# Performance work log

Measured on AMD Instinct MI355X. Metric: run time of the kernel, lower is better.

## Reference

```python
import jax, jax.numpy as jnp
import numpy as np

B, S, D, H, DC, HC, M = 2, 2048, 1024, 16, 64, 16, 4096
DH = D // H  # head_dim = 64


def _ln(x, g, b, eps=1e-5):
    m = jnp.mean(x, axis=-1, keepdims=True)
    v = jnp.var(x, axis=-1, keepdims=True)
    return (x - m) * jax.lax.rsqrt(v + eps) * g + b


def setup_inputs() -> dict:
    key = jax.random.key(0)
    ks = jax.random.split(key, 10)
    def w(k, shape, fan_in):
        return jax.random.normal(k, shape, jnp.float32) * (fan_in ** -0.5)
    return {
        "h": jax.random.normal(ks[0], (B, S, D), jnp.float32),
        "z": jax.random.normal(ks[1], (B, S, DC), jnp.float32),
        # Linear weights stored [in, out] (transpose of torch layout)
        "wv": w(ks[2], (D, D), D),   "bv": jnp.zeros((D,), jnp.float32),
        "wca": w(ks[3], (DC, H * HC), DC), "bca": jnp.zeros((H * HC,), jnp.float32),
        "wcn": w(ks[4], (D, DC), D), "bcn": jnp.zeros((DC,), jnp.float32),
        "wo": w(ks[5], (D, D), D),   "bo": jnp.zeros((D,), jnp.float32),
        "gamma": jnp.zeros((1, H, 1, 1), jnp.float32),
        "w1": w(ks[6], (D, M), D),   "b1": jnp.zeros((M,), jnp.float32),
        "w2": w(ks[7], (M, D), M),   "b2": jnp.zeros((D,), jnp.float32),
        "ln1_g": jnp.ones((D,), jnp.float32),  "ln1_b": jnp.zeros((D,), jnp.float32),
        "ln2_g": jnp.ones((D,), jnp.float32),  "ln2_b": jnp.zeros((D,), jnp.float32),
        "lnc_g": jnp.ones((DC,), jnp.float32), "lnc_b": jnp.zeros((DC,), jnp.float32),
    }


def reference(h, z, wv, bv, wca, bca, wcn, bcn, wo, bo, gamma,
              w1, b1, w2, b2, ln1_g, ln1_b, ln2_g, ln2_b, lnc_g, lnc_b):
    hn = _ln(h, ln1_g, ln1_b)
    # values: [B,S,H,DH]
    value = (hn @ wv + bv).reshape(B, S, H, DH)
    # per-head coordinates: [B,S,H,HC]
    zh = (z @ wca + bca).reshape(B, S, H, HC)
    # pairwise squared distances per head: ||zq||^2 + ||zk||^2 - 2 zq.zk
    z_sq = jnp.sum(zh * zh, axis=-1).transpose(0, 2, 1)        # [B,H,S]
    dot = jnp.einsum('bqhc,bkhc->bhqk', zh, zh)                # [B,H,S,S]
    sq_dist = jnp.maximum(z_sq[:, :, :, None] + z_sq[:, :, None, :] - 2.0 * dot, 0.0)
    g = jax.nn.softplus(gamma)                                 # [1,H,1,1]
    attn = jax.nn.softmax(-g * sq_dist, axis=-1)               # [B,H,S,S]
    attn_out = jnp.einsum('bhqk,bkhd->bqhd', attn, value).reshape(B, S, D)
    h_attn = attn_out @ wo + bo
    z_next = hn @ wcn + bcn
    h = h + h_attn
    # FFN (dropout is identity in eval); torch GELU default is exact (erf)
    hn2 = _ln(h, ln2_g, ln2_b)
    ffn = jax.nn.gelu(hn2 @ w1 + b1, approximate=False) @ w2 + b2
    h = h + ffn
    z_out = _ln(z + z_next, lnc_g, lnc_b)
    return h, z_out
```

## Files before the change

### kernel.cpp

```cpp
#include <hip/hip_runtime.h>

#define USH unsigned short

__device__ __forceinline__ float b2f(USH u) {
    union { unsigned int i; float f; } x; x.i = ((unsigned int)u) << 16; return x.f;
}
__device__ __forceinline__ USH f2b(float f) {
    union { float f; unsigned int i; } x; x.f = f;
    unsigned int r = x.i + (0x7fffu + ((x.i >> 16) & 1u));
    return (USH)(r >> 16);
}
__device__ __forceinline__ float ldf(const USH* p)  { return b2f(*p); }
__device__ __forceinline__ float ldf(const float* p){ return *p; }
__device__ __forceinline__ void stf(USH* p, float v)  { *p = f2b(v); }
__device__ __forceinline__ void stf(float* p, float v){ *p = v; }

#define GLOAD16(gp, lp) __builtin_amdgcn_global_load_lds(                     \
    (const __attribute__((address_space(1))) void*)(gp),                      \
    (__attribute__((address_space(3))) void*)(lp), 16, 0, 0)

typedef __attribute__((ext_vector_type(8))) __bf16 bf16x8;
typedef __attribute__((ext_vector_type(4))) float  floatx4;

__global__ __launch_bounds__(256) void transpose_f2b(const float* __restrict__ W,
                                                     USH* __restrict__ WT,
                                                     int K, int N) {
    __shared__ USH t[64][72];
    int n0 = blockIdx.x * 64, k0 = blockIdx.y * 64;
    int tid = threadIdx.x;
    int kr = tid >> 4, nc = (tid & 15) * 4;
#pragma unroll
    for (int r = 0; r < 4; r++) {
        int k = kr + r * 16;
        float4 v = *(const float4*)(W + (size_t)(k0 + k) * N + n0 + nc);
        t[nc + 0][k] = f2b(v.x); t[nc + 1][k] = f2b(v.y);
        t[nc + 2][k] = f2b(v.z); t[nc + 3][k] = f2b(v.w);
    }
    __syncthreads();
    int nr = tid >> 2, kc = (tid & 3) * 8;
#pragma unroll
    for (int r = 0; r < 2; r++) {
        int k = kc + r * 32;
        *(int4*)(WT + (size_t)(n0 + nr) * K + k0 + k) = *(const int4*)&t[nr][k];
    }
}

template <typename TX>
__global__ __launch_bounds__(256) void ln_rows(const TX* __restrict__ x,
                                               const float* __restrict__ g,
                                               const float* __restrict__ bb,
                                               USH* __restrict__ y) {
    int row = blockIdx.x, tid = threadIdx.x;
    const TX* xr = x + (size_t)row * 1024 + tid * 4;
    float v[4];
#pragma unroll
    for (int i = 0; i < 4; i++) v[i] = ldf(xr + i);
    float s  = v[0] + v[1] + v[2] + v[3];
    float ss = v[0]*v[0] + v[1]*v[1] + v[2]*v[2] + v[3]*v[3];
#pragma unroll
    for (int o = 32; o; o >>= 1) { s += __shfl_down(s, o); ss += __shfl_down(ss, o); }
    __shared__ float red[10];
    int w = tid >> 6;
    if ((tid & 63) == 0) { red[w] = s; red[4 + w] = ss; }
    __syncthreads();
    if (tid == 0) {
        float S = red[0] + red[1] + red[2] + red[3];
        float SS = red[4] + red[5] + red[6] + red[7];
        float mean = S * (1.f / 1024.f);
        float var  = SS * (1.f / 1024.f) - mean * mean;
        red[8] = mean; red[9] = rsqrtf(var + 1e-5f);
    }
    __syncthreads();
    float mean = red[8], rstd = red[9];
    USH* yr = y + (size_t)row * 1024 + tid * 4;
#pragma unroll
    for (int i = 0; i < 4; i++) {
        int c = tid * 4 + i;
        yr[i] = f2b((v[i] - mean) * rstd * g[c] + bb[c]);
    }
}

__global__ __launch_bounds__(256) void zh_kernel(const float* __restrict__ z,
                                                 const float* __restrict__ wca,
                                                 const float* __restrict__ bca,
                                                 const float* __restrict__ gamma,
                                                 USH* __restrict__ zq_pack,
                                                 USH* __restrict__ zk_pack) {
    int row = blockIdx.x, n = threadIdx.x;
    __shared__ float zrow[64];
    if (n < 64) zrow[n] = z[(size_t)row * 64 + n];
    __syncthreads();
    float s = bca[n];
#pragma unroll 8
    for (int k = 0; k < 64; k++) s = fmaf(zrow[k], wca[(size_t)k * 256 + n], s);
    int h = n >> 4, c = n & 15;
    float gvl = log1pf(__expf(gamma[h])) * 1.44269504f;
    USH u = f2b(s);
    float sv = b2f(u);
    float sq = sv * sv;
    sq += __shfl_xor(sq, 1); sq += __shfl_xor(sq, 2);
    sq += __shfl_xor(sq, 4); sq += __shfl_xor(sq, 8);
    size_t base = ((size_t)h * 4096 + row) * 32;
    zk_pack[base + c] = u;
    zq_pack[base + c] = f2b(2.f * gvl * s);
    if (c == 0) {
        USH hi = f2b(sq);
        float lo = sq - b2f(hi);
        unsigned int kw0 = 0x3F80u | ((unsigned int)hi << 16);
        unsigned int kw1 = (unsigned int)f2b(lo);
        uint4 kv = {kw0, kw1, 0u, 0u};
        uint4 zz = {0u, 0u, 0u, 0u};
        *(uint4*)(zk_pack + base + 16) = kv;
        *(uint4*)(zk_pack + base + 24) = zz;
        unsigned int qw0 = (unsigned int)f2b(-gvl * sq) | ((unsigned int)f2b(-gvl) << 16);
        unsigned int qw1 = (unsigned int)f2b(-gvl);
        uint4 qv = {qw0, qw1, 0u, 0u};
        *(uint4*)(zq_pack + base + 16) = qv;
        *(uint4*)(zq_pack + base + 24) = zz;
    }
}

template <int EPI, int MI, int NI, int KB, typename TRES, typename TOUT>
__global__ __launch_bounds__(256) void gemm_kernel(const USH* __restrict__ A,
                                                   const USH* __restrict__ WT,
                                                   const float* __restrict__ bias,
                                                   const TRES* __restrict__ res,
                                                   TOUT* __restrict__ out,
                                                   int M, int N, int K) {
    constexpr int BM  = MI * 32;
    constexpr int BN  = NI * 32;
    constexpr int GR  = KB / 8;
    constexpr int RPC = 2048 / KB;
    constexpr int ACH = BM / RPC;
    constexpr int BCH = BN / RPC;
    __shared__ __align__(16) USH lA[BM][KB];
    __shared__ __align__(16) USH lB[BN][KB];
    int tid = threadIdx.x;
    int lane = tid & 63, wave = tid >> 6;
    int wr = wave >> 1, wc = wave & 1;
    int quad = lane >> 4, l15 = lane & 15;
    int m0 = blockIdx.x * BM, n0 = blockIdx.y * BN;

    int srow = tid / GR;
    int kg   = tid % GR;
    int scol = (kg ^ (srow & 7)) * 8;

    const USH* gA = A + (size_t)(m0 + srow) * K + scol;
    const USH* gB = WT + (size_t)(n0 + srow) * K + scol;
    USH* lA0 = &lA[0][0] + tid * 8;
    USH* lB0 = &lB[0][0] + tid * 8;
    int xo = (l15 & 7) * 8;

    floatx4 acc[MI][NI] = {};

    for (int k0 = 0; k0 < K; k0 += KB) {
#pragma unroll
        for (int c = 0; c < ACH; c++)
            GLOAD16(gA + (size_t)c * RPC * K + k0, lA0 + c * 2048);
#pragma unroll
        for (int c = 0; c < BCH; c++)
            GLOAD16(gB + (size_t)c * RPC * K + k0, lB0 + c * 2048);
        __syncthreads();

#pragma unroll
        for (int ks = 0; ks < KB / 32; ks++) {
            bf16x8 bfr[NI];
#pragma unroll
            for (int ni = 0; ni < NI; ni++)
                bfr[ni] = *(const bf16x8*)&lB[wc * (NI * 16) + ni * 16 + l15][(ks * 32 + quad * 8) ^ xo];
#pragma unroll
            for (int mi = 0; mi < MI; mi++) {
                bf16x8 afr = *(const bf16x8*)&lA[wr * (MI * 16) + mi * 16 + l15][(ks * 32 + quad * 8) ^ xo];
#pragma unroll
                for (int ni = 0; ni < NI; ni++)
                    acc[mi][ni] = __builtin_amdgcn_mfma_f32_16x16x32_bf16(afr, bfr[ni], acc[mi][ni], 0, 0, 0);
            }
        }
        __syncthreads();
    }

    float bias_v[NI];
#pragma unroll
    for (int ni = 0; ni < NI; ni++) bias_v[ni] = bias[n0 + wc * (NI * 16) + ni * 16 + l15];

#pragma unroll
    for (int mi = 0; mi < MI; mi++) {
#pragma unroll
        for (int r = 0; r < 4; r++) {
            int row = m0 + wr * (MI * 16) + mi * 16 + quad * 4 + r;
            size_t base = (size_t)row * N;
#pragma unroll
            for (int ni = 0; ni < NI; ni++) {
                int col = n0 + wc * (NI * 16) + ni * 16 + l15;
                float v = acc[mi][ni][r] + bias_v[ni];
                if (EPI == 2) {
                    float t = v * v;
                    float a = fmaf(t, -0.0713548162726f, -1.59576912161f);
                    v = v * __builtin_amdgcn_rcpf(1.f + __expf(v * a));
                }
                if (EPI == 1 || EPI == 3) v += ldf(res + base + col);
                stf(out + base + col, v);
            }
        }
    }
}

__global__ __launch_bounds__(512) void attn11_kernel(const USH* __restrict__ zq_pack,
                                                     const USH* __restrict__ zk_pack,
                                                     const USH* __restrict__ value,
                                                     USH* __restrict__ attn_out) {
    int b = blockIdx.x >> 4, h = blockIdx.x & 15;
    int q0 = blockIdx.y * 128;
    int tid = threadIdx.x, lane = tid & 63, wq = tid >> 6;
    int quad = lane >> 4, l15 = lane & 15;

    __shared__ __align__(16) USH Qb[128][40];
    __shared__ __align__(16) USH KbT[2][64][40];
    __shared__ __align__(16) USH VbT[2][64][72];
    __shared__ __align__(16) USH Pb[8][16][72];

    const size_t zrow0 = (size_t)b * 2048;
    const USH* zq = zq_pack + ((size_t)h * 4096 + zrow0) * 32;
    const USH* zk = zk_pack + ((size_t)h * 4096 + zrow0) * 32;
    const size_t vbase = zrow0 * 1024 + h * 64;

    {
        int row = tid >> 2, c0 = (tid & 3) * 8;
        *(uint4*)&Qb[row][c0] = *(const uint4*)(zq + (size_t)(q0 + row) * 32 + c0);
    }
    __syncthreads();

    bf16x8 afragQ = *(const bf16x8*)&Qb[wq * 16 + l15][quad * 8];

    union { unsigned int u[4]; bf16x8 v; } onesu;
#pragma unroll
    for (int i = 0; i < 4; i++) onesu.u[i] = 0x3F803F80u;
    bf16x8 ones = onesu.v;

    floatx4 oacc[4] = {};
    floatx4 lacc = {};

    int kp  = tid & 31;
    int va  = kp & 15, vb = kp >> 4;
    int vrow = va + vb * 32;
    int dh0  = (tid >> 5) * 8;
    int cb   = va * 4 + vb * 2;
    int krow = (tid - 256) >> 2, kc0 = ((tid - 256) & 3) * 8;
    int4 vta, vtb; uint4 kreg;

    if (tid < 256) {
        const USH* s0 = value + vbase + (size_t)vrow * 1024 + dh0;
        vta = *(const int4*)s0;
        vtb = *(const int4*)(s0 + 16 * 1024);
        const USH* ua = (const USH*)&vta;
        const USH* ub = (const USH*)&vtb;
#pragma unroll
        for (int e = 0; e < 8; e++) {
            unsigned int dw = (unsigned int)ua[e] | ((unsigned int)ub[e] << 16);
            *(unsigned int*)&VbT[0][dh0 + e][cb] = dw;
        }
        const USH* s1 = value + vbase + (size_t)(64 + vrow) * 1024 + dh0;
        vta = *(const int4*)s1;
        vtb = *(const int4*)(s1 + 16 * 1024);
    } else {
        kreg = *(const uint4*)(zk + (size_t)krow * 32 + kc0);
        *(uint4*)&KbT[0][krow][kc0] = kreg;
        kreg = *(const uint4*)(zk + (size_t)(64 + krow) * 32 + kc0);
    }

    for (int it = 0; it < 32; it++) {
        int cur = it & 1;
        __syncthreads();
        if (it + 1 < 32) {
            if (tid < 256) {
                const USH* ua = (const USH*)&vta;
                const USH* ub = (const USH*)&vtb;
#pragma unroll
                for (int e = 0; e < 8; e++) {
                    unsigned int dw = (unsigned int)ua[e] | ((unsigned int)ub[e] << 16);
                    *(unsigned int*)&VbT[cur ^ 1][dh0 + e][cb] = dw;
                }
                if (it + 2 < 32) {
                    const USH* s0 = value + vbase + (size_t)((it + 2) * 64 + vrow) * 1024 + dh0;
                    vta = *(const int4*)s0;
                    vtb = *(const int4*)(s0 + 16 * 1024);
                }
            } else {
                *(uint4*)&KbT[cur ^ 1][krow][kc0] = kreg;
                if (it + 2 < 32)
                    kreg = *(const uint4*)(zk + (size_t)((it + 2) * 64 + krow) * 32 + kc0);
            }
        }

        bf16x8 bk[4];
#pragma unroll
        for (int ni = 0; ni < 4; ni++)
            bk[ni] = *(const bf16x8*)&KbT[cur][ni * 16 + l15][quad * 8];

        floatx4 sacc[4];
#pragma unroll
        for (int ni = 0; ni < 4; ni++) {
            floatx4 zz = {};
            sacc[ni] = __builtin_amdgcn_mfma_f32_16x16x32_bf16(afragQ, bk[ni], zz, 0, 0, 0);
        }

#pragma unroll
        for (int r = 0; r < 4; r++) {
            union { float f; unsigned int i; } c0, c1, c2, c3;
            c0.f = exp2f(sacc[0][r]); c1.f = exp2f(sacc[1][r]);
            c2.f = exp2f(sacc[2][r]); c3.f = exp2f(sacc[3][r]);
            uint2 dw;
            dw.x = (c0.i >> 16) | (c1.i & 0xFFFF0000u);
            dw.y = (c2.i >> 16) | (c3.i & 0xFFFF0000u);
            *(uint2*)&Pb[wq][quad * 4 + r][l15 * 4] = dw;
        }

#pragma unroll
        for (int ks2 = 0; ks2 < 2; ks2++) {
            bf16x8 bv[4];
#pragma unroll
            for (int nd = 0; nd < 4; nd++)
                bv[nd] = *(const bf16x8*)&VbT[cur][nd * 16 + l15][ks2 * 32 + quad * 8];
            bf16x8 ap = *(const bf16x8*)&Pb[wq][l15][ks2 * 32 + quad * 8];
#pragma unroll
            for (int nd = 0; nd < 4; nd++)
                oacc[nd] = __builtin_amdgcn_mfma_f32_16x16x32_bf16(ap, bv[nd], oacc[nd], 0, 0, 0);
            lacc = __builtin_amdgcn_mfma_f32_16x16x32_bf16(ap, ones, lacc, 0, 0, 0);
        }
    }

#pragma unroll
    for (int r = 0; r < 4; r++) {
        float inv = 1.f / lacc[r];
        int row = q0 + wq * 16 + quad * 4 + r;
        USH* o = attn_out + (zrow0 + row) * 1024 + h * 64;
#pragma unroll
        for (int nd = 0; nd < 4; nd++) o[nd * 16 + l15] = f2b(oacc[nd][r] * inv);
    }
}

__global__ __launch_bounds__(64) void lnc_kernel(const float* __restrict__ z,
                                                 const float* __restrict__ zn,
                                                 const float* __restrict__ g,
                                                 const float* __restrict__ bb,
                                                 float* __restrict__ out) {
    int row = blockIdx.x, t = threadIdx.x;
    float v = z[(size_t)row * 64 + t] + zn[(size_t)row * 64 + t];
    float s = v, ss = v * v;
#pragma unroll
    for (int o = 32; o; o >>= 1) { s += __shfl_xor(s, o); ss += __shfl_xor(ss, o); }
    float mean = s * (1.f / 64.f);
    float rstd = rsqrtf(ss * (1.f / 64.f) - mean * mean + 1e-5f);
    out[(size_t)row * 64 + t] = (v - mean) * rstd * g[t] + bb[t];
}

extern "C" void kernel_launch(void* const* d_in, const int* in_sizes, int n_in,
                              void* d_out, int out_size, void* d_ws, size_t ws_size,
                              hipStream_t stream) {
    char* p = (char*)d_ws;
    USH*   value   = (USH*)(p);
    USH*   attn_o  = (USH*)(p + ((size_t)8  << 20));
    USH*   wcnT    = (USH*)(p + ((size_t)8  << 20));
    USH*   zq_pack = (USH*)(p + ((size_t)16 << 20));
    USH*   zk_pack = (USH*)(p + ((size_t)20 << 20));
    USH*   hn      = (USH*)(p + ((size_t)24 << 20));
    USH*   mid     = (USH*)(p);
    USH*   hn2     = (USH*)(p + ((size_t)32 << 20));
    float* znext   = (float*)(p + ((size_t)40 << 20));
    USH*   wvT     = (USH*)(p + ((size_t)41 << 20));
    USH*   woT     = (USH*)(p + ((size_t)43 << 20));
    USH*   w1T     = (USH*)(p + ((size_t)45 << 20));
    USH*   w2T     = (USH*)(p + ((size_t)53 << 20));

    const float *h    = (const float*)d_in[0],  *z    = (const float*)d_in[1];
    const float *wv   = (const float*)d_in[2],  *bv   = (const float*)d_in[3];
    const float *wca  = (const float*)d_in[4],  *bca  = (const float*)d_in[5];
    const float *wcn  = (const float*)d_in[6],  *bcn  = (const float*)d_in[7];
    const float *wo   = (const float*)d_in[8],  *bo   = (const float*)d_in[9];
    const float *gam  = (const float*)d_in[10];
    const float *w1   = (const float*)d_in[11], *b1   = (const float*)d_in[12];
    const float *w2   = (const float*)d_in[13], *b2   = (const float*)d_in[14];
    const float *ln1g = (const float*)d_in[15], *ln1b = (const float*)d_in[16];
    const float *ln2g = (const float*)d_in[17], *ln2b = (const float*)d_in[18];
    const float *lncg = (const float*)d_in[19], *lncb = (const float*)d_in[20];

    float* out_h = (float*)d_out;
    float* out_z = out_h + (size_t)4096 * 1024;
    float* h1    = out_h;

    transpose_f2b<<<dim3(16, 16), 256, 0, stream>>>(wv, wvT, 1024, 1024);
    transpose_f2b<<<dim3(16, 16), 256, 0, stream>>>(wo, woT, 1024, 1024);
    transpose_f2b<<<dim3(64, 16), 256, 0, stream>>>(w1, w1T, 1024, 4096);
    transpose_f2b<<<dim3(16, 64), 256, 0, stream>>>(w2, w2T, 4096, 1024);
    transpose_f2b<<<dim3(1, 16),  256, 0, stream>>>(wcn, wcnT, 1024, 64);

    ln_rows<float><<<4096, 256, 0, stream>>>(h, ln1g, ln1b, hn);
    zh_kernel<<<4096, 256, 0, stream>>>(z, wca, bca, gam, zq_pack, zk_pack);
    gemm_kernel<0, 4, 2, 128, USH, USH><<<dim3(32, 16), 256, 0, stream>>>(hn, wvT, bv, (const USH*)nullptr, value, 4096, 1024, 1024);
    gemm_kernel<0, 1, 1, 64, float, float><<<dim3(128, 2), 256, 0, stream>>>(hn, wcnT, bcn, (const float*)nullptr, znext, 4096, 64, 1024);
    attn11_kernel<<<dim3(32, 16), 512, 0, stream>>>(zq_pack, zk_pack, value, attn_o);
    gemm_kernel<1, 4, 2, 128, float, float><<<dim3(32, 16), 256, 0, stream>>>(attn_o, woT, bo, h, h1, 4096, 1024, 1024);
    ln_rows<float><<<4096, 256, 0, stream>>>(h1, ln2g, ln2b, hn2);
    gemm_kernel<2, 4, 4, 64, USH, USH><<<dim3(32, 32), 256, 0, stream>>>(hn2, w1T, b1, (const USH*)nullptr, mid, 4096, 4096, 1024);
    gemm_kernel<3, 4, 2, 128, float, float><<<dim3(32, 16), 256, 0, stream>>>(mid, w2T, b2, h1, out_h, 4096, 1024, 4096);
    lnc_kernel<<<4096, 64, 0, stream>>>(z, znext, lncg, lncb, out_z);
}
```

Baseline: 353.9 us.

## Split attention key tiles across warp groups and merge partial sums in LDS

The attention kernel now handles 64 queries per block instead of 128, doubling the grid. Within each block, two warp groups each process half of every 64-key tile, and their partial output and denominator accumulators are summed through shared memory at the end. The V transpose layout is changed to match, and shared memory is reused for the merge buffer. The aim is more blocks to fill the CUs and shorter dependent MFMA chains per wave. The cost is that each query block streams K and V from global memory, so total K/V loading doubles, plus an extra LDS reduction step.

```diff
diff --git a/kernel.cpp b/kernel.cpp
--- a/kernel.cpp
+++ b/kernel.cpp
@@ -205,32 +205,31 @@
     }
 }
 
-__global__ __launch_bounds__(512) void attn11_kernel(const USH* __restrict__ zq_pack,
+__global__ __launch_bounds__(512) void attn12_kernel(const USH* __restrict__ zq_pack,
                                                      const USH* __restrict__ zk_pack,
                                                      const USH* __restrict__ value,
                                                      USH* __restrict__ attn_out) {
     int b = blockIdx.x >> 4, h = blockIdx.x & 15;
-    int q0 = blockIdx.y * 128;
+    int q0 = blockIdx.y * 64;
     int tid = threadIdx.x, lane = tid & 63, wq = tid >> 6;
+    int qw = wq & 3, kg = wq >> 2;
     int quad = lane >> 4, l15 = lane & 15;
 
-    __shared__ __align__(16) USH Qb[128][40];
-    __shared__ __align__(16) USH KbT[2][64][40];
-    __shared__ __align__(16) USH VbT[2][64][72];
-    __shared__ __align__(16) USH Pb[8][16][72];
+    __shared__ __align__(16) char smem[38912];
+    typedef USH VbT_t[64][72];
+    typedef USH KbT_t[64][40];
+    typedef USH Pb_t[16][40];
+    VbT_t* VbT = reinterpret_cast<VbT_t*>(smem);
+    KbT_t* KbT = reinterpret_cast<KbT_t*>(smem + 18432);
+    Pb_t*  Pb  = reinterpret_cast<Pb_t*>(smem + 28672);
+    float (*mrg)[21] = reinterpret_cast<float(*)[21]>(smem);
 
     const size_t zrow0 = (size_t)b * 2048;
     const USH* zq = zq_pack + ((size_t)h * 4096 + zrow0) * 32;
     const USH* zk = zk_pack + ((size_t)h * 4096 + zrow0) * 32;
     const size_t vbase = zrow0 * 1024 + h * 64;
 
-    {
-        int row = tid >> 2, c0 = (tid & 3) * 8;
-        *(uint4*)&Qb[row][c0] = *(const uint4*)(zq + (size_t)(q0 + row) * 32 + c0);
-    }
-    __syncthreads();
-
-    bf16x8 afragQ = *(const bf16x8*)&Qb[wq * 16 + l15][quad * 8];
+    bf16x8 afragQ = *(const bf16x8*)(zq + (size_t)(q0 + qw * 16 + l15) * 32 + quad * 8);
 
     union { unsigned int u[4]; bf16x8 v; } onesu;
 #pragma unroll
@@ -240,11 +239,11 @@
     floatx4 oacc[4] = {};
     floatx4 lacc = {};
 
-    int kp  = tid & 31;
-    int va  = kp & 15, vb = kp >> 4;
+    int kp   = tid & 31;
+    int va   = kp & 15, vb = kp >> 4;
     int vrow = va + vb * 32;
     int dh0  = (tid >> 5) * 8;
-    int cb   = va * 4 + vb * 2;
+    int cb   = vb * 32 + va * 2;
     int krow = (tid - 256) >> 2, kc0 = ((tid - 256) & 3) * 8;
     int4 vta, vtb; uint4 kreg;
 
@@ -292,50 +291,56 @@
             }
         }
 
-        bf16x8 bk[4];
-#pragma unroll
-        for (int ni = 0; ni < 4; ni++)
-            bk[ni] = *(const bf16x8*)&KbT[cur][ni * 16 + l15][quad * 8];
-
-        floatx4 sacc[4];
-#pragma unroll
-        for (int ni = 0; ni < 4; ni++) {
-            floatx4 zz = {};
-            sacc[ni] = __builtin_amdgcn_mfma_f32_16x16x32_bf16(afragQ, bk[ni], zz, 0, 0, 0);
-        }
+        bf16x8 bk0 = *(const bf16x8*)&KbT[cur][(kg * 2 + 0) * 16 + l15][quad * 8];
+        bf16x8 bk1 = *(const bf16x8*)&KbT[cur][(kg * 2 + 1) * 16 + l15][quad * 8];
+        floatx4 z0 = {}, z1 = {};
+        floatx4 s0 = __builtin_amdgcn_mfma_f32_16x16x32_bf16(afragQ, bk0, z0, 0, 0, 0);
+        floatx4 s1 = __builtin_amdgcn_mfma_f32_16x16x32_bf16(afragQ, bk1, z1, 0, 0, 0);
 
 #pragma unroll
         for (int r = 0; r < 4; r++) {
-            union { float f; unsigned int i; } c0, c1, c2, c3;
-            c0.f = exp2f(sacc[0][r]); c1.f = exp2f(sacc[1][r]);
-            c2.f = exp2f(sacc[2][r]); c3.f = exp2f(sacc[3][r]);
-            uint2 dw;
-            dw.x = (c0.i >> 16) | (c1.i & 0xFFFF0000u);
-            dw.y = (c2.i >> 16) | (c3.i & 0xFFFF0000u);
-            *(uint2*)&Pb[wq][quad * 4 + r][l15 * 4] = dw;
-        }
-
-#pragma unroll
-        for (int ks2 = 0; ks2 < 2; ks2++) {
-            bf16x8 bv[4];
-#pragma unroll
-            for (int nd = 0; nd < 4; nd++)
-                bv[nd] = *(const bf16x8*)&VbT[cur][nd * 16 + l15][ks2 * 32 + quad * 8];
-            bf16x8 ap = *(const bf16x8*)&Pb[wq][l15][ks2 * 32 + quad * 8];
-#pragma unroll
-            for (int nd = 0; nd < 4; nd++)
-                oacc[nd] = __builtin_amdgcn_mfma_f32_16x16x32_bf16(ap, bv[nd], oacc[nd], 0, 0, 0);
-            lacc = __builtin_amdgcn_mfma_f32_16x16x32_bf16(ap, ones, lacc, 0, 0, 0);
-        }
-    }
-
-#pragma unroll
-    for (int r = 0; r < 4; r++) {
-        float inv = 1.f / lacc[r];
-        int row = q0 + wq * 16 + quad * 4 + r;
-        USH* o = attn_out + (zrow0 + row) * 1024 + h * 64;
-#pragma unroll
-        for (int nd = 0; nd < 4; nd++) o[nd * 16 + l15] = f2b(oacc[nd][r] * inv);
+            union { float f; unsigned int i; } c0, c1;
+            c0.f = exp2f(s0[r]); c1.f = exp2f(s1[r]);
+            unsigned int dw = (c0.i >> 16) | (c1.i & 0xFFFF0000u);
+            *(unsigned int*)&Pb[wq][quad * 4 + r][l15 * 2] = dw;
+        }
+
+        bf16x8 bv[4];
+#pragma unroll
+        for (int nd = 0; nd < 4; nd++)
+            bv[nd] = *(const bf16x8*)&VbT[cur][nd * 16 + l15][kg * 32 + quad * 8];
+        bf16x8 ap = *(const bf16x8*)&Pb[wq][l15][quad * 8];
+#pragma unroll
+        for (int nd = 0; nd < 4; nd++)
+            oacc[nd] = __builtin_amdgcn_mfma_f32_16x16x32_bf16(ap, bv[nd], oacc[nd], 0, 0, 0);
+        lacc = __builtin_amdgcn_mfma_f32_16x16x32_bf16(ap, ones, lacc, 0, 0, 0);
+    }
+
+    __syncthreads();
+    if (kg == 1) {
+        float* m = mrg[qw * 64 + lane];
+#pragma unroll
+        for (int nd = 0; nd < 4; nd++)
+#pragma unroll
+            for (int r = 0; r < 4; r++) m[nd * 4 + r] = oacc[nd][r];
+#pragma unroll
+        for (int r = 0; r < 4; r++) m[16 + r] = lacc[r];
+    }
+    __syncthreads();
+    if (kg == 0) {
+        const float* m = mrg[qw * 64 + lane];
+#pragma unroll
+        for (int nd = 0; nd < 4; nd++)
+#pragma unroll
+            for (int r = 0; r < 4; r++) oacc[nd][r] += m[nd * 4 + r];
+#pragma unroll
+        for (int r = 0; r < 4; r++) {
+            float inv = 1.f / (lacc[r] + m[16 + r]);
+            int row = q0 + qw * 16 + quad * 4 + r;
+            USH* o = attn_out + (zrow0 + row) * 1024 + h * 64;
+#pragma unroll
+            for (int nd = 0; nd < 4; nd++) o[nd * 16 + l15] = f2b(oacc[nd][r] * inv);
+        }
     }
 }
 
@@ -398,7 +403,7 @@
     zh_kernel<<<4096, 256, 0, stream>>>(z, wca, bca, gam, zq_pack, zk_pack);
     gemm_kernel<0, 4, 2, 128, USH, USH><<<dim3(32, 16), 256, 0, stream>>>(hn, wvT, bv, (const USH*)nullptr, value, 4096, 1024, 1024);
     gemm_kernel<0, 1, 1, 64, float, float><<<dim3(128, 2), 256, 0, stream>>>(hn, wcnT, bcn, (const float*)nullptr, znext, 4096, 64, 1024);
-    attn11_kernel<<<dim3(32, 16), 512, 0, stream>>>(zq_pack, zk_pack, value, attn_o);
+    attn12_kernel<<<dim3(32, 32), 512, 0, stream>>>(zq_pack, zk_pack, value, attn_o);
     gemm_kernel<1, 4, 2, 128, float, float><<<dim3(32, 16), 256, 0, stream>>>(attn_o, woT, bo, h, h1, 4096, 1024, 1024);
     ln_rows<float><<<4096, 256, 0, stream>>>(h1, ln2g, ln2b, hn2);
     gemm_kernel<2, 4, 4, 64, USH, USH><<<dim3(32, 32), 256, 0, stream>>>(hn2, w1T, b1, (const USH*)nullptr, mid, 4096, 4096, 1024);
```

New measurement: 362.9 us. 1.03x slower.
